# Kernel tuning notes

Hardware: AMD Instinct MI355X
Metric: run time of the kernel (lower is better)

## Reference

```python
import jax, jax.numpy as jnp
import numpy as np

B, H, S, D = 2, 12, 2048, 64

def setup_inputs() -> dict:
    key = jax.random.key(0)
    kq, kk, kv, km = jax.random.split(key, 4)
    return {
        "q": jax.random.normal(kq, (B, H, S, D), dtype=jnp.float32),
        "k": jax.random.normal(kk, (B, H, S, D), dtype=jnp.float32),
        "v": jax.random.normal(kv, (B, H, S, D), dtype=jnp.float32),
        "mask": jax.random.normal(km, (B, 1, S, S), dtype=jnp.float32),
    }

def reference(q, k, v, mask):
    # scores: [B,H,S,S] = Q @ K^T + mask (additive, broadcast over heads)
    scores = jnp.einsum("bhqd,bhkd->bhqk", q, k) + mask
    probs = jax.nn.softmax(scores, axis=-1)
    return jnp.einsum("bhqk,bhkd->bhqd", probs, v)
```

## Files before the change

### kernel.cpp

```cpp
#include <hip/hip_runtime.h>
#include <hip/hip_bf16.h>
#include <stdint.h>

#define S_LEN 2048
#define D_DIM 64
#define HEADS 12
#define KVB   64
#define QBLK  64
#define NTILES (S_LEN / KVB)
#define BH    (2 * HEADS)
#define TILE_BYTES 8192
#define KH_OFF ((size_t)0)
#define KL_OFF ((size_t)BH * NTILES * TILE_BYTES)
#define VT_OFF ((size_t)2 * BH * NTILES * TILE_BYTES)
#define WS_NEED ((size_t)3 * BH * NTILES * TILE_BYTES)

typedef __attribute__((ext_vector_type(8))) short bf16x8;
typedef __attribute__((ext_vector_type(4))) float f32x4;

__device__ __forceinline__ unsigned short f2bf(float x) {
    union { float f; uint32_t u; } v; v.f = x;
    uint32_t r = v.u + 0x7FFFu + ((v.u >> 16) & 1u);
    return (unsigned short)(r >> 16);
}
__device__ __forceinline__ float bf2f(unsigned short h) {
    union { uint32_t u; float f; } t; t.u = ((uint32_t)h) << 16; return t.f;
}
__device__ __forceinline__ void split2(float x, unsigned short& h, unsigned short& l) {
    h = f2bf(x);
    l = f2bf(x - bf2f(h));
}
__device__ __forceinline__ void gload16(const void* g, void* l) {
    __builtin_amdgcn_global_load_lds(
        (const __attribute__((address_space(1))) void*)g,
        (__attribute__((address_space(3))) void*)l, 16, 0, 0);
}

__global__ __launch_bounds__(256, 4)
void convert_kv(const float* __restrict__ K, const float* __restrict__ V,
                unsigned char* __restrict__ ws)
{
    const int blk = blockIdx.x;
    const int bh  = blk >> 5;
    const int t   = blk & 31;
    const long qkv_base = (long)bh * S_LEN * D_DIM;
    const int tid = threadIdx.x;
    unsigned char* kh = ws + KH_OFF + (size_t)blk * TILE_BYTES;
    unsigned char* kl = ws + KL_OFF + (size_t)blk * TILE_BYTES;
    unsigned char* vt = ws + VT_OFF + (size_t)blk * TILE_BYTES;
    const int k0 = t * KVB;

    const float* kp = K + qkv_base + (long)k0 * D_DIM;
    #pragma unroll
    for (int it = 0; it < 4; ++it) {
        int i   = tid + 256 * it;
        int row = i >> 4;
        int c4  = i & 15;
        float4 x = *(const float4*)(kp + row * 64 + c4 * 4);
        unsigned short h0, l0, h1, l1, h2, l2, h3, l3;
        split2(x.x, h0, l0); split2(x.y, h1, l1);
        split2(x.z, h2, l2); split2(x.w, h3, l3);
        int off = row * 128 + ((c4 * 8) ^ ((row & 7) << 4));
        *(uint2*)(kh + off) = make_uint2(((uint32_t)h1 << 16) | h0, ((uint32_t)h3 << 16) | h2);
        *(uint2*)(kl + off) = make_uint2(((uint32_t)l1 << 16) | l0, ((uint32_t)l3 << 16) | l2);
    }

    const float* vp = V + qkv_base + (long)k0 * D_DIM;
    int d = tid & 63, a = tid >> 6;
    #pragma unroll
    for (int h = 0; h < 2; ++h) {
        int kk0 = 32 * h + 8 * a;
        float e0 = vp[(kk0 + 0) * 64 + d], e1 = vp[(kk0 + 1) * 64 + d];
        float e2 = vp[(kk0 + 2) * 64 + d], e3 = vp[(kk0 + 3) * 64 + d];
        float e4 = vp[(kk0 + 4) * 64 + d], e5 = vp[(kk0 + 5) * 64 + d];
        float e6 = vp[(kk0 + 6) * 64 + d], e7 = vp[(kk0 + 7) * 64 + d];
        uint32_t w0 = ((uint32_t)f2bf(e1) << 16) | f2bf(e0);
        uint32_t w1 = ((uint32_t)f2bf(e3) << 16) | f2bf(e2);
        uint32_t w2 = ((uint32_t)f2bf(e5) << 16) | f2bf(e4);
        uint32_t w3 = ((uint32_t)f2bf(e7) << 16) | f2bf(e6);
        int off = d * 128 + ((kk0 * 2) ^ ((d & 7) << 4));
        *(uint4*)(vt + off) = make_uint4(w0, w1, w2, w3);
    }
}

__global__ __launch_bounds__(256, 3)
void attn_fwd_ws(const float* __restrict__ Q, const float* __restrict__ M,
                 const unsigned char* __restrict__ ws, float* __restrict__ O)
{
    __shared__ unsigned char klds_h[8192];
    __shared__ unsigned char klds_l[8192];
    __shared__ unsigned char vlds[8192];
    __shared__ unsigned char mlds[16384];

    const int bid  = blockIdx.x;
    const int bh   = bid >> 5;
    const int qb   = bid & 31;
    const int b    = bh / HEADS;
    const long qkv_base  = (long)bh * S_LEN * D_DIM;
    const long mask_base = (long)b * S_LEN * S_LEN;

    const int tid  = threadIdx.x;
    const int wave = tid >> 6;
    const int lane = tid & 63;
    const int c    = lane & 15;
    const int g    = lane >> 4;
    const int sw   = (c & 7) << 4;

    const int qrow = qb * QBLK + wave * 16 + c;

    bf16x8 qfh[2], qfl[2];
    {
        const float* qp = Q + qkv_base + (long)qrow * D_DIM;
        #pragma unroll
        for (int f = 0; f < 2; ++f) {
            float4 x0 = *(const float4*)(qp + f * 32 + 8 * g);
            float4 x1 = *(const float4*)(qp + f * 32 + 8 * g + 4);
            float e[8] = { x0.x, x0.y, x0.z, x0.w, x1.x, x1.y, x1.z, x1.w };
            bf16x8 th, tl;
            #pragma unroll
            for (int j = 0; j < 8; ++j) {
                unsigned short h, l;
                split2(e[j], h, l);
                th[j] = (short)h; tl[j] = (short)l;
            }
            qfh[f] = th; qfl[f] = tl;
        }
    }

    const unsigned char* khB = ws + KH_OFF + (size_t)bh * NTILES * TILE_BYTES;
    const unsigned char* klB = ws + KL_OFF + (size_t)bh * NTILES * TILE_BYTES;
    const unsigned char* vtB = ws + VT_OFF + (size_t)bh * NTILES * TILE_BYTES;
    const float* mrow0 = M + mask_base + (long)(qb * QBLK) * S_LEN;

    f32x4 o[4] = {};
    float m_run = -INFINITY, l_run = 0.f;

    for (int t0 = 0; t0 < NTILES; ++t0) {
        const unsigned char* khT = khB + (size_t)t0 * TILE_BYTES;
        const unsigned char* klT = klB + (size_t)t0 * TILE_BYTES;
        const unsigned char* vtT = vtB + (size_t)t0 * TILE_BYTES;

        #pragma unroll
        for (int j = 0; j < 2; ++j) {
            int o2 = wave * 2048 + j * 1024;
            gload16(khT + o2 + lane * 16, klds_h + o2);
            gload16(klT + o2 + lane * 16, klds_l + o2);
            gload16(vtT + o2 + lane * 16, vlds + o2);
        }
        #pragma unroll
        for (int j = 0; j < 4; ++j) {
            int o2 = wave * 4096 + j * 1024;
            int X  = o2 + lane * 16;
            int q  = X >> 8;
            int ib = X & 255;
            const unsigned char* gm =
                (const unsigned char*)(mrow0 + (long)q * S_LEN) + t0 * 256;
            gload16(gm + (ib ^ ((q & 7) << 4)), mlds + o2);
        }
        __syncthreads();

        f32x4 st[4];
        #pragma unroll
        for (int kt = 0; kt < 4; ++kt) {
            const unsigned char* bh_ = klds_h + (16 * kt + c) * 128;
            const unsigned char* bl_ = klds_l + (16 * kt + c) * 128;
            bf16x8 kh0 = *(const bf16x8*)(bh_ + ((16 * g) ^ sw));
            bf16x8 kh1 = *(const bf16x8*)(bh_ + ((64 + 16 * g) ^ sw));
            bf16x8 kl0 = *(const bf16x8*)(bl_ + ((16 * g) ^ sw));
            bf16x8 kl1 = *(const bf16x8*)(bl_ + ((64 + 16 * g) ^ sw));
            f32x4 acc = {};
            acc = __builtin_amdgcn_mfma_f32_16x16x32_bf16(kh0, qfl[0], acc, 0, 0, 0);
            acc = __builtin_amdgcn_mfma_f32_16x16x32_bf16(kh1, qfl[1], acc, 0, 0, 0);
            acc = __builtin_amdgcn_mfma_f32_16x16x32_bf16(kl0, qfh[0], acc, 0, 0, 0);
            acc = __builtin_amdgcn_mfma_f32_16x16x32_bf16(kl1, qfh[1], acc, 0, 0, 0);
            acc = __builtin_amdgcn_mfma_f32_16x16x32_bf16(kh0, qfh[0], acc, 0, 0, 0);
            acc = __builtin_amdgcn_mfma_f32_16x16x32_bf16(kh1, qfh[1], acc, 0, 0, 0);
            st[kt] = acc;
        }

        const int mq = wave * 16 + c;
        const unsigned char* mrl = mlds + mq * 256;
        float p[4][4];
        float tmax = -INFINITY;
        #pragma unroll
        for (int kt = 0; kt < 4; ++kt) {
            union { float4 v; float a[4]; } mu;
            mu.v = *(const float4*)(mrl + ((64 * kt + 16 * g) ^ sw));
            #pragma unroll
            for (int r = 0; r < 4; ++r) {
                float sc = st[kt][r] + mu.a[r];
                p[kt][r] = sc;
                tmax = fmaxf(tmax, sc);
            }
        }
        tmax = fmaxf(tmax, __shfl_xor(tmax, 16, 64));
        tmax = fmaxf(tmax, __shfl_xor(tmax, 32, 64));
        float m_new = fmaxf(m_run, tmax);
        float scale = __expf(m_run - m_new);
        float tsum = 0.f;
        #pragma unroll
        for (int kt = 0; kt < 4; ++kt)
            #pragma unroll
            for (int r = 0; r < 4; ++r) {
                float e = __expf(p[kt][r] - m_new);
                p[kt][r] = e;
                tsum += e;
            }
        tsum += __shfl_xor(tsum, 16, 64);
        tsum += __shfl_xor(tsum, 32, 64);
        l_run = l_run * scale + tsum;
        m_run = m_new;
        #pragma unroll
        for (int mt = 0; mt < 4; ++mt) o[mt] *= scale;

        uint32_t w[4][2];
        #pragma unroll
        for (int kt = 0; kt < 4; ++kt) {
            w[kt][0] = ((uint32_t)f2bf(p[kt][1]) << 16) | f2bf(p[kt][0]);
            w[kt][1] = ((uint32_t)f2bf(p[kt][3]) << 16) | f2bf(p[kt][2]);
        }
        bf16x8 pf[2];
        const bool hi_half = (lane & 32) != 0;
        #pragma unroll
        for (int f = 0; f < 2; ++f) {
            uint32_t words[4];
            #pragma unroll
            for (int pp = 0; pp < 4; ++pp) {
                int srcl = 16 * (2 * (g & 1) + (pp >> 1)) + c;
                int addr = srcl << 2;
                int lo = __builtin_amdgcn_ds_bpermute(addr, (int)w[2 * f][pp & 1]);
                int hi = __builtin_amdgcn_ds_bpermute(addr, (int)w[2 * f + 1][pp & 1]);
                words[pp] = hi_half ? (uint32_t)hi : (uint32_t)lo;
            }
            union { uint32_t u[4]; bf16x8 v; } cv;
            cv.u[0] = words[0]; cv.u[1] = words[1];
            cv.u[2] = words[2]; cv.u[3] = words[3];
            pf[f] = cv.v;
        }

        #pragma unroll
        for (int f = 0; f < 2; ++f) {
            #pragma unroll
            for (int mt = 0; mt < 4; ++mt) {
                const unsigned char* base = vlds + (16 * mt + c) * 128;
                bf16x8 vf = *(const bf16x8*)(base + ((64 * f + 16 * g) ^ sw));
                o[mt] = __builtin_amdgcn_mfma_f32_16x16x32_bf16(vf, pf[f], o[mt], 0, 0, 0);
            }
        }
        __syncthreads();
    }

    float inv = 1.0f / l_run;
    float* op = O + qkv_base + (long)qrow * D_DIM;
    #pragma unroll
    for (int mt = 0; mt < 4; ++mt) {
        float4 x = make_float4(o[mt][0] * inv, o[mt][1] * inv,
                               o[mt][2] * inv, o[mt][3] * inv);
        *(float4*)(op + 16 * mt + 4 * g) = x;
    }
}

__global__ __launch_bounds__(256, 3)
void attn_fwd(const float* __restrict__ Q, const float* __restrict__ K,
              const float* __restrict__ V, const float* __restrict__ M,
              float* __restrict__ O)
{
    __shared__ unsigned char klds_h[64 * 128];
    __shared__ unsigned char klds_l[64 * 128];
    __shared__ unsigned char vlds[64 * 128];

    const int bid  = blockIdx.x;
    const int bh   = bid >> 5;
    const int qb   = bid & 31;
    const int b    = bh / HEADS;
    const long qkv_base  = (long)bh * S_LEN * D_DIM;
    const long mask_base = (long)b * S_LEN * S_LEN;

    const int tid  = threadIdx.x;
    const int wave = tid >> 6;
    const int lane = tid & 63;
    const int c    = lane & 15;
    const int g    = lane >> 4;
    const int sw   = (c & 7) << 4;

    const int qrow = qb * QBLK + wave * 16 + c;

    bf16x8 qfh[2], qfl[2];
    {
        const float* qp = Q + qkv_base + (long)qrow * D_DIM;
        #pragma unroll
        for (int f = 0; f < 2; ++f) {
            float4 x0 = *(const float4*)(qp + f * 32 + 8 * g);
            float4 x1 = *(const float4*)(qp + f * 32 + 8 * g + 4);
            float e[8] = { x0.x, x0.y, x0.z, x0.w, x1.x, x1.y, x1.z, x1.w };
            bf16x8 th, tl;
            #pragma unroll
            for (int j = 0; j < 8; ++j) {
                unsigned short h, l;
                split2(e[j], h, l);
                th[j] = (short)h; tl[j] = (short)l;
            }
            qfh[f] = th; qfl[f] = tl;
        }
    }

    f32x4 o[4] = {};
    float m_run = -INFINITY, l_run = 0.f;
    const float* mrow = M + mask_base + (long)qrow * S_LEN;

    for (int t0 = 0; t0 < NTILES; ++t0) {
        const int k0 = t0 * KVB;
        {
            const float* kp = K + qkv_base + (long)k0 * D_DIM;
            #pragma unroll
            for (int it = 0; it < 4; ++it) {
                int i   = tid + 256 * it;
                int row = i >> 4;
                int c4  = i & 15;
                float4 x = *(const float4*)(kp + row * 64 + c4 * 4);
                unsigned short h0, l0, h1, l1, h2, l2, h3, l3;
                split2(x.x, h0, l0); split2(x.y, h1, l1);
                split2(x.z, h2, l2); split2(x.w, h3, l3);
                int off = row * 128 + ((c4 * 8) ^ ((row & 7) << 4));
                *(uint2*)(klds_h + off) =
                    make_uint2(((uint32_t)h1 << 16) | h0, ((uint32_t)h3 << 16) | h2);
                *(uint2*)(klds_l + off) =
                    make_uint2(((uint32_t)l1 << 16) | l0, ((uint32_t)l3 << 16) | l2);
            }
        }
        {
            const float* vp = V + qkv_base + (long)k0 * D_DIM;
            int d = tid & 63, a = tid >> 6;
            #pragma unroll
            for (int h = 0; h < 2; ++h) {
                int kk0 = 32 * h + 8 * a;
                float e0 = vp[(kk0 + 0) * 64 + d], e1 = vp[(kk0 + 1) * 64 + d];
                float e2 = vp[(kk0 + 2) * 64 + d], e3 = vp[(kk0 + 3) * 64 + d];
                float e4 = vp[(kk0 + 4) * 64 + d], e5 = vp[(kk0 + 5) * 64 + d];
                float e6 = vp[(kk0 + 6) * 64 + d], e7 = vp[(kk0 + 7) * 64 + d];
                uint32_t w0 = ((uint32_t)f2bf(e1) << 16) | f2bf(e0);
                uint32_t w1 = ((uint32_t)f2bf(e3) << 16) | f2bf(e2);
                uint32_t w2 = ((uint32_t)f2bf(e5) << 16) | f2bf(e4);
                uint32_t w3 = ((uint32_t)f2bf(e7) << 16) | f2bf(e6);
                int off = d * 128 + ((kk0 * 2) ^ ((d & 7) << 4));
                *(uint4*)(vlds + off) = make_uint4(w0, w1, w2, w3);
            }
        }
        __syncthreads();

        f32x4 st[4];
        #pragma unroll
        for (int kt = 0; kt < 4; ++kt) {
            const unsigned char* bh_ = klds_h + (16 * kt + c) * 128;
            const unsigned char* bl_ = klds_l + (16 * kt + c) * 128;
            bf16x8 kh0 = *(const bf16x8*)(bh_ + ((16 * g) ^ sw));
            bf16x8 kh1 = *(const bf16x8*)(bh_ + ((64 + 16 * g) ^ sw));
            bf16x8 kl0 = *(const bf16x8*)(bl_ + ((16 * g) ^ sw));
            bf16x8 kl1 = *(const bf16x8*)(bl_ + ((64 + 16 * g) ^ sw));
            f32x4 acc = {};
            acc = __builtin_amdgcn_mfma_f32_16x16x32_bf16(kh0, qfl[0], acc, 0, 0, 0);
            acc = __builtin_amdgcn_mfma_f32_16x16x32_bf16(kh1, qfl[1], acc, 0, 0, 0);
            acc = __builtin_amdgcn_mfma_f32_16x16x32_bf16(kl0, qfh[0], acc, 0, 0, 0);
            acc = __builtin_amdgcn_mfma_f32_16x16x32_bf16(kl1, qfh[1], acc, 0, 0, 0);
            acc = __builtin_amdgcn_mfma_f32_16x16x32_bf16(kh0, qfh[0], acc, 0, 0, 0);
            acc = __builtin_amdgcn_mfma_f32_16x16x32_bf16(kh1, qfh[1], acc, 0, 0, 0);
            st[kt] = acc;
        }

        float p[4][4];
        float tmax = -INFINITY;
        #pragma unroll
        for (int kt = 0; kt < 4; ++kt)
            #pragma unroll
            for (int r = 0; r < 4; ++r) {
                float sc = st[kt][r] + mrow[k0 + 16 * kt + 4 * g + r];
                p[kt][r] = sc;
                tmax = fmaxf(tmax, sc);
            }
        tmax = fmaxf(tmax, __shfl_xor(tmax, 16, 64));
        tmax = fmaxf(tmax, __shfl_xor(tmax, 32, 64));
        float m_new = fmaxf(m_run, tmax);
        float scale = __expf(m_run - m_new);
        float tsum = 0.f;
        #pragma unroll
        for (int kt = 0; kt < 4; ++kt)
            #pragma unroll
            for (int r = 0; r < 4; ++r) {
                float e = __expf(p[kt][r] - m_new);
                p[kt][r] = e;
                tsum += e;
            }
        tsum += __shfl_xor(tsum, 16, 64);
        tsum += __shfl_xor(tsum, 32, 64);
        l_run = l_run * scale + tsum;
        m_run = m_new;
        #pragma unroll
        for (int mt = 0; mt < 4; ++mt) o[mt] *= scale;

        uint32_t w[4][2];
        #pragma unroll
        for (int kt = 0; kt < 4; ++kt) {
            w[kt][0] = ((uint32_t)f2bf(p[kt][1]) << 16) | f2bf(p[kt][0]);
            w[kt][1] = ((uint32_t)f2bf(p[kt][3]) << 16) | f2bf(p[kt][2]);
        }
        bf16x8 pf[2];
        const bool hi_half = (lane & 32) != 0;
        #pragma unroll
        for (int f = 0; f < 2; ++f) {
            uint32_t words[4];
            #pragma unroll
            for (int pp = 0; pp < 4; ++pp) {
                int srcl = 16 * (2 * (g & 1) + (pp >> 1)) + c;
                int addr = srcl << 2;
                int lo = __builtin_amdgcn_ds_bpermute(addr, (int)w[2 * f][pp & 1]);
                int hi = __builtin_amdgcn_ds_bpermute(addr, (int)w[2 * f + 1][pp & 1]);
                words[pp] = hi_half ? (uint32_t)hi : (uint32_t)lo;
            }
            union { uint32_t u[4]; bf16x8 v; } cv;
            cv.u[0] = words[0]; cv.u[1] = words[1];
            cv.u[2] = words[2]; cv.u[3] = words[3];
            pf[f] = cv.v;
        }

        #pragma unroll
        for (int f = 0; f < 2; ++f) {
            #pragma unroll
            for (int mt = 0; mt < 4; ++mt) {
                const unsigned char* base = vlds + (16 * mt + c) * 128;
                bf16x8 vf = *(const bf16x8*)(base + ((64 * f + 16 * g) ^ sw));
                o[mt] = __builtin_amdgcn_mfma_f32_16x16x32_bf16(vf, pf[f], o[mt], 0, 0, 0);
            }
        }
        __syncthreads();
    }

    float inv = 1.0f / l_run;
    float* op = O + qkv_base + (long)qrow * D_DIM;
    #pragma unroll
    for (int mt = 0; mt < 4; ++mt) {
        float4 x = make_float4(o[mt][0] * inv, o[mt][1] * inv,
                               o[mt][2] * inv, o[mt][3] * inv);
        *(float4*)(op + 16 * mt + 4 * g) = x;
    }
}

extern "C" void kernel_launch(void* const* d_in, const int* in_sizes, int n_in,
                              void* d_out, int out_size, void* d_ws, size_t ws_size,
                              hipStream_t stream) {
    const float* q = (const float*)d_in[0];
    const float* k = (const float*)d_in[1];
    const float* v = (const float*)d_in[2];
    const float* m = (const float*)d_in[3];
    float* o = (float*)d_out;
    dim3 grid(BH * (S_LEN / QBLK));
    dim3 block(256);
    if (ws_size >= WS_NEED) {
        convert_kv<<<grid, block, 0, stream>>>(k, v, (unsigned char*)d_ws);
        attn_fwd_ws<<<grid, block, 0, stream>>>(q, m, (const unsigned char*)d_ws, o);
    } else {
        attn_fwd<<<grid, block, 0, stream>>>(q, k, v, m, o);
    }
}
```

Baseline: 195.2 us.

## Double-buffer K/V tiles in LDS and prefetch mask rows into registers

The main attention kernel now double-buffers the K-high, K-low and V tiles in LDS, issuing the async global-to-LDS loads for tile t+1 before computing tile t. This hides load latency and leaves one barrier per iteration. The mask is no longer staged through a swizzled LDS buffer; each lane reads its own row directly into registers one tile ahead. The convert kernel now stages results in LDS and writes them out as coalesced 16-byte stores. The trade-off is more LDS (48KB vs 40KB) and more registers, which may lower occupancy, and mask reads are now strided per lane.

```diff
diff --git a/kernel.cpp b/kernel.cpp
--- a/kernel.cpp
+++ b/kernel.cpp
@@ -40,14 +40,15 @@
 void convert_kv(const float* __restrict__ K, const float* __restrict__ V,
                 unsigned char* __restrict__ ws)
 {
+    __shared__ unsigned char kh_s[8192];
+    __shared__ unsigned char kl_s[8192];
+    __shared__ unsigned char vt_s[8192];
+
     const int blk = blockIdx.x;
     const int bh  = blk >> 5;
     const int t   = blk & 31;
     const long qkv_base = (long)bh * S_LEN * D_DIM;
     const int tid = threadIdx.x;
-    unsigned char* kh = ws + KH_OFF + (size_t)blk * TILE_BYTES;
-    unsigned char* kl = ws + KL_OFF + (size_t)blk * TILE_BYTES;
-    unsigned char* vt = ws + VT_OFF + (size_t)blk * TILE_BYTES;
     const int k0 = t * KVB;
 
     const float* kp = K + qkv_base + (long)k0 * D_DIM;
@@ -61,8 +62,8 @@
         split2(x.x, h0, l0); split2(x.y, h1, l1);
         split2(x.z, h2, l2); split2(x.w, h3, l3);
         int off = row * 128 + ((c4 * 8) ^ ((row & 7) << 4));
-        *(uint2*)(kh + off) = make_uint2(((uint32_t)h1 << 16) | h0, ((uint32_t)h3 << 16) | h2);
-        *(uint2*)(kl + off) = make_uint2(((uint32_t)l1 << 16) | l0, ((uint32_t)l3 << 16) | l2);
+        *(uint2*)(kh_s + off) = make_uint2(((uint32_t)h1 << 16) | h0, ((uint32_t)h3 << 16) | h2);
+        *(uint2*)(kl_s + off) = make_uint2(((uint32_t)l1 << 16) | l0, ((uint32_t)l3 << 16) | l2);
     }
 
     const float* vp = V + qkv_base + (long)k0 * D_DIM;
@@ -79,18 +80,43 @@
         uint32_t w2 = ((uint32_t)f2bf(e5) << 16) | f2bf(e4);
         uint32_t w3 = ((uint32_t)f2bf(e7) << 16) | f2bf(e6);
         int off = d * 128 + ((kk0 * 2) ^ ((d & 7) << 4));
-        *(uint4*)(vt + off) = make_uint4(w0, w1, w2, w3);
+        *(uint4*)(vt_s + off) = make_uint4(w0, w1, w2, w3);
+    }
+    __syncthreads();
+
+    unsigned char* kh = ws + KH_OFF + (size_t)blk * TILE_BYTES;
+    unsigned char* kl = ws + KL_OFF + (size_t)blk * TILE_BYTES;
+    unsigned char* vt = ws + VT_OFF + (size_t)blk * TILE_BYTES;
+    #pragma unroll
+    for (int i = 0; i < 2; ++i) {
+        int X = tid * 16 + i * 4096;
+        *(uint4*)(kh + X) = *(const uint4*)(kh_s + X);
+        *(uint4*)(kl + X) = *(const uint4*)(kl_s + X);
+        *(uint4*)(vt + X) = *(const uint4*)(vt_s + X);
+    }
+}
+
+__device__ __forceinline__ void stage_tiles(const unsigned char* khT, const unsigned char* klT,
+                                            const unsigned char* vtT,
+                                            unsigned char* kh_d, unsigned char* kl_d,
+                                            unsigned char* vt_d, int wave, int lane)
+{
+    #pragma unroll
+    for (int j = 0; j < 2; ++j) {
+        int o2 = wave * 2048 + j * 1024;
+        gload16(khT + o2 + lane * 16, kh_d + o2);
+        gload16(klT + o2 + lane * 16, kl_d + o2);
+        gload16(vtT + o2 + lane * 16, vt_d + o2);
     }
 }
 
 __global__ __launch_bounds__(256, 3)
-void attn_fwd_ws(const float* __restrict__ Q, const float* __restrict__ M,
+void attn_fwd_db(const float* __restrict__ Q, const float* __restrict__ M,
                  const unsigned char* __restrict__ ws, float* __restrict__ O)
 {
-    __shared__ unsigned char klds_h[8192];
-    __shared__ unsigned char klds_l[8192];
-    __shared__ unsigned char vlds[8192];
-    __shared__ unsigned char mlds[16384];
+    __shared__ unsigned char klds_h[2][8192];
+    __shared__ unsigned char klds_l[2][8192];
+    __shared__ unsigned char vlds[2][8192];
 
     const int bid  = blockIdx.x;
     const int bh   = bid >> 5;
@@ -130,32 +156,215 @@
     const unsigned char* khB = ws + KH_OFF + (size_t)bh * NTILES * TILE_BYTES;
     const unsigned char* klB = ws + KL_OFF + (size_t)bh * NTILES * TILE_BYTES;
     const unsigned char* vtB = ws + VT_OFF + (size_t)bh * NTILES * TILE_BYTES;
-    const float* mrow0 = M + mask_base + (long)(qb * QBLK) * S_LEN;
+    const float* mrow = M + mask_base + (long)qrow * S_LEN;
 
     f32x4 o[4] = {};
     float m_run = -INFINITY, l_run = 0.f;
 
+    stage_tiles(khB, klB, vtB, klds_h[0], klds_l[0], vlds[0], wave, lane);
+    f32x4 mreg[4], nreg[4];
+    #pragma unroll
+    for (int kt = 0; kt < 4; ++kt)
+        mreg[kt] = *(const f32x4*)(mrow + 16 * kt + 4 * g);
+    __syncthreads();
+
+    int cur = 0;
     for (int t0 = 0; t0 < NTILES; ++t0) {
-        const unsigned char* khT = khB + (size_t)t0 * TILE_BYTES;
-        const unsigned char* klT = klB + (size_t)t0 * TILE_BYTES;
-        const unsigned char* vtT = vtB + (size_t)t0 * TILE_BYTES;
-
-        #pragma unroll
-        for (int j = 0; j < 2; ++j) {
-            int o2 = wave * 2048 + j * 1024;
-            gload16(khT + o2 + lane * 16, klds_h + o2);
-            gload16(klT + o2 + lane * 16, klds_l + o2);
-            gload16(vtT + o2 + lane * 16, vlds + o2);
-        }
-        #pragma unroll
-        for (int j = 0; j < 4; ++j) {
-            int o2 = wave * 4096 + j * 1024;
-            int X  = o2 + lane * 16;
-            int q  = X >> 8;
-            int ib = X & 255;
-            const unsigned char* gm =
-                (const unsigned char*)(mrow0 + (long)q * S_LEN) + t0 * 256;
-            gload16(gm + (ib ^ ((q & 7) << 4)), mlds + o2);
+        if (t0 + 1 < NTILES) {
+            stage_tiles(khB + (size_t)(t0 + 1) * TILE_BYTES,
+                        klB + (size_t)(t0 + 1) * TILE_BYTES,
+                        vtB + (size_t)(t0 + 1) * TILE_BYTES,
+                        klds_h[cur ^ 1], klds_l[cur ^ 1], vlds[cur ^ 1], wave, lane);
+            #pragma unroll
+            for (int kt = 0; kt < 4; ++kt)
+                nreg[kt] = *(const f32x4*)(mrow + (t0 + 1) * 64 + 16 * kt + 4 * g);
+        }
+
+        f32x4 st[4];
+        #pragma unroll
+        for (int kt = 0; kt < 4; ++kt) {
+            const unsigned char* bh_ = klds_h[cur] + (16 * kt + c) * 128;
+            const unsigned char* bl_ = klds_l[cur] + (16 * kt + c) * 128;
+            bf16x8 kh0 = *(const bf16x8*)(bh_ + ((16 * g) ^ sw));
+            bf16x8 kh1 = *(const bf16x8*)(bh_ + ((64 + 16 * g) ^ sw));
+            bf16x8 kl0 = *(const bf16x8*)(bl_ + ((16 * g) ^ sw));
+            bf16x8 kl1 = *(const bf16x8*)(bl_ + ((64 + 16 * g) ^ sw));
+            f32x4 acc = {};
+            acc = __builtin_amdgcn_mfma_f32_16x16x32_bf16(kh0, qfl[0], acc, 0, 0, 0);
+            acc = __builtin_amdgcn_mfma_f32_16x16x32_bf16(kh1, qfl[1], acc, 0, 0, 0);
+            acc = __builtin_amdgcn_mfma_f32_16x16x32_bf16(kl0, qfh[0], acc, 0, 0, 0);
+            acc = __builtin_amdgcn_mfma_f32_16x16x32_bf16(kl1, qfh[1], acc, 0, 0, 0);
+            acc = __builtin_amdgcn_mfma_f32_16x16x32_bf16(kh0, qfh[0], acc, 0, 0, 0);
+            acc = __builtin_amdgcn_mfma_f32_16x16x32_bf16(kh1, qfh[1], acc, 0, 0, 0);
+            st[kt] = acc;
+        }
+
+        float p[4][4];
+        float tmax = -INFINITY;
+        #pragma unroll
+        for (int kt = 0; kt < 4; ++kt)
+            #pragma unroll
+            for (int r = 0; r < 4; ++r) {
+                float sc = st[kt][r] + mreg[kt][r];
+                p[kt][r] = sc;
+                tmax = fmaxf(tmax, sc);
+            }
+        tmax = fmaxf(tmax, __shfl_xor(tmax, 16, 64));
+        tmax = fmaxf(tmax, __shfl_xor(tmax, 32, 64));
+        float m_new = fmaxf(m_run, tmax);
+        float scale = __expf(m_run - m_new);
+        float tsum = 0.f;
+        #pragma unroll
+        for (int kt = 0; kt < 4; ++kt)
+            #pragma unroll
+            for (int r = 0; r < 4; ++r) {
+                float e = __expf(p[kt][r] - m_new);
+                p[kt][r] = e;
+                tsum += e;
+            }
+        tsum += __shfl_xor(tsum, 16, 64);
+        tsum += __shfl_xor(tsum, 32, 64);
+        l_run = l_run * scale + tsum;
+        m_run = m_new;
+        #pragma unroll
+        for (int mt = 0; mt < 4; ++mt) o[mt] *= scale;
+
+        uint32_t w[4][2];
+        #pragma unroll
+        for (int kt = 0; kt < 4; ++kt) {
+            w[kt][0] = ((uint32_t)f2bf(p[kt][1]) << 16) | f2bf(p[kt][0]);
+            w[kt][1] = ((uint32_t)f2bf(p[kt][3]) << 16) | f2bf(p[kt][2]);
+        }
+        bf16x8 pf[2];
+        const bool hi_half = (lane & 32) != 0;
+        #pragma unroll
+        for (int f = 0; f < 2; ++f) {
+            uint32_t words[4];
+            #pragma unroll
+            for (int pp = 0; pp < 4; ++pp) {
+                int srcl = 16 * (2 * (g & 1) + (pp >> 1)) + c;
+                int addr = srcl << 2;
+                int lo = __builtin_amdgcn_ds_bpermute(addr, (int)w[2 * f][pp & 1]);
+                int hi = __builtin_amdgcn_ds_bpermute(addr, (int)w[2 * f + 1][pp & 1]);
+                words[pp] = hi_half ? (uint32_t)hi : (uint32_t)lo;
+            }
+            union { uint32_t u[4]; bf16x8 v; } cv;
+            cv.u[0] = words[0]; cv.u[1] = words[1];
+            cv.u[2] = words[2]; cv.u[3] = words[3];
+            pf[f] = cv.v;
+        }
+
+        #pragma unroll
+        for (int f = 0; f < 2; ++f) {
+            #pragma unroll
+            for (int mt = 0; mt < 4; ++mt) {
+                const unsigned char* base = vlds[cur] + (16 * mt + c) * 128;
+                bf16x8 vf = *(const bf16x8*)(base + ((64 * f + 16 * g) ^ sw));
+                o[mt] = __builtin_amdgcn_mfma_f32_16x16x32_bf16(vf, pf[f], o[mt], 0, 0, 0);
+            }
+        }
+
+        __syncthreads();
+        cur ^= 1;
+        #pragma unroll
+        for (int kt = 0; kt < 4; ++kt) mreg[kt] = nreg[kt];
+    }
+
+    float inv = 1.0f / l_run;
+    float* op = O + qkv_base + (long)qrow * D_DIM;
+    #pragma unroll
+    for (int mt = 0; mt < 4; ++mt) {
+        float4 x = make_float4(o[mt][0] * inv, o[mt][1] * inv,
+                               o[mt][2] * inv, o[mt][3] * inv);
+        *(float4*)(op + 16 * mt + 4 * g) = x;
+    }
+}
+
+__global__ __launch_bounds__(256, 3)
+void attn_fwd(const float* __restrict__ Q, const float* __restrict__ K,
+              const float* __restrict__ V, const float* __restrict__ M,
+              float* __restrict__ O)
+{
+    __shared__ unsigned char klds_h[64 * 128];
+    __shared__ unsigned char klds_l[64 * 128];
+    __shared__ unsigned char vlds[64 * 128];
+
+    const int bid  = blockIdx.x;
+    const int bh   = bid >> 5;
+    const int qb   = bid & 31;
+    const int b    = bh / HEADS;
+    const long qkv_base  = (long)bh * S_LEN * D_DIM;
+    const long mask_base = (long)b * S_LEN * S_LEN;
+
+    const int tid  = threadIdx.x;
+    const int wave = tid >> 6;
+    const int lane = tid & 63;
+    const int c    = lane & 15;
+    const int g    = lane >> 4;
+    const int sw   = (c & 7) << 4;
+
+    const int qrow = qb * QBLK + wave * 16 + c;
+
+    bf16x8 qfh[2], qfl[2];
+    {
+        const float* qp = Q + qkv_base + (long)qrow * D_DIM;
+        #pragma unroll
+        for (int f = 0; f < 2; ++f) {
+            float4 x0 = *(const float4*)(qp + f * 32 + 8 * g);
+            float4 x1 = *(const float4*)(qp + f * 32 + 8 * g + 4);
+            float e[8] = { x0.x, x0.y, x0.z, x0.w, x1.x, x1.y, x1.z, x1.w };
+            bf16x8 th, tl;
+            #pragma unroll
+            for (int j = 0; j < 8; ++j) {
+                unsigned short h, l;
+                split2(e[j], h, l);
+                th[j] = (short)h; tl[j] = (short)l;
+            }
+            qfh[f] = th; qfl[f] = tl;
+        }
+    }
+
+    f32x4 o[4] = {};
+    float m_run = -INFINITY, l_run = 0.f;
+    const float* mrow = M + mask_base + (long)qrow * S_LEN;
+
+    for (int t0 = 0; t0 < NTILES; ++t0) {
+        const int k0 = t0 * KVB;
+        {
+            const float* kp = K + qkv_base + (long)k0 * D_DIM;
+            #pragma unroll
+            for (int it = 0; it < 4; ++it) {
+                int i   = tid + 256 * it;
+                int row = i >> 4;
+                int c4  = i & 15;
+                float4 x = *(const float4*)(kp + row * 64 + c4 * 4);
+                unsigned short h0, l0, h1, l1, h2, l2, h3, l3;
+                split2(x.x, h0, l0); split2(x.y, h1, l1);
+                split2(x.z, h2, l2); split2(x.w, h3, l3);
+                int off = row * 128 + ((c4 * 8) ^ ((row & 7) << 4));
+                *(uint2*)(klds_h + off) =
+                    make_uint2(((uint32_t)h1 << 16) | h0, ((uint32_t)h3 << 16) | h2);
+                *(uint2*)(klds_l + off) =
+                    make_uint2(((uint32_t)l1 << 16) | l0, ((uint32_t)l3 << 16) | l2);
+            }
+        }
+        {
+            const float* vp = V + qkv_base + (long)k0 * D_DIM;
+            int d = tid & 63, a = tid >> 6;
+            #pragma unroll
+            for (int h = 0; h < 2; ++h) {
+                int kk0 = 32 * h + 8 * a;
+                float e0 = vp[(kk0 + 0) * 64 + d], e1 = vp[(kk0 + 1) * 64 + d];
+                float e2 = vp[(kk0 + 2) * 64 + d], e3 = vp[(kk0 + 3) * 64 + d];
+                float e4 = vp[(kk0 + 4) * 64 + d], e5 = vp[(kk0 + 5) * 64 + d];
+                float e6 = vp[(kk0 + 6) * 64 + d], e7 = vp[(kk0 + 7) * 64 + d];
+                uint32_t w0 = ((uint32_t)f2bf(e1) << 16) | f2bf(e0);
+                uint32_t w1 = ((uint32_t)f2bf(e3) << 16) | f2bf(e2);
+                uint32_t w2 = ((uint32_t)f2bf(e5) << 16) | f2bf(e4);
+                uint32_t w3 = ((uint32_t)f2bf(e7) << 16) | f2bf(e6);
+                int off = d * 128 + ((kk0 * 2) ^ ((d & 7) << 4));
+                *(uint4*)(vlds + off) = make_uint4(w0, w1, w2, w3);
+            }
         }
         __syncthreads();
 
@@ -178,195 +387,6 @@
             st[kt] = acc;
         }
 
-        const int mq = wave * 16 + c;
-        const unsigned char* mrl = mlds + mq * 256;
-        float p[4][4];
-        float tmax = -INFINITY;
-        #pragma unroll
-        for (int kt = 0; kt < 4; ++kt) {
-            union { float4 v; float a[4]; } mu;
-            mu.v = *(const float4*)(mrl + ((64 * kt + 16 * g) ^ sw));
-            #pragma unroll
-            for (int r = 0; r < 4; ++r) {
-                float sc = st[kt][r] + mu.a[r];
-                p[kt][r] = sc;
-                tmax = fmaxf(tmax, sc);
-            }
-        }
-        tmax = fmaxf(tmax, __shfl_xor(tmax, 16, 64));
-        tmax = fmaxf(tmax, __shfl_xor(tmax, 32, 64));
-        float m_new = fmaxf(m_run, tmax);
-        float scale = __expf(m_run - m_new);
-        float tsum = 0.f;
-        #pragma unroll
-        for (int kt = 0; kt < 4; ++kt)
-            #pragma unroll
-            for (int r = 0; r < 4; ++r) {
-                float e = __expf(p[kt][r] - m_new);
-                p[kt][r] = e;
-                tsum += e;
-            }
-        tsum += __shfl_xor(tsum, 16, 64);
-        tsum += __shfl_xor(tsum, 32, 64);
-        l_run = l_run * scale + tsum;
-        m_run = m_new;
-        #pragma unroll
-        for (int mt = 0; mt < 4; ++mt) o[mt] *= scale;
-
-        uint32_t w[4][2];
-        #pragma unroll
-        for (int kt = 0; kt < 4; ++kt) {
-            w[kt][0] = ((uint32_t)f2bf(p[kt][1]) << 16) | f2bf(p[kt][0]);
-            w[kt][1] = ((uint32_t)f2bf(p[kt][3]) << 16) | f2bf(p[kt][2]);
-        }
-        bf16x8 pf[2];
-        const bool hi_half = (lane & 32) != 0;
-        #pragma unroll
-        for (int f = 0; f < 2; ++f) {
-            uint32_t words[4];
-            #pragma unroll
-            for (int pp = 0; pp < 4; ++pp) {
-                int srcl = 16 * (2 * (g & 1) + (pp >> 1)) + c;
-                int addr = srcl << 2;
-                int lo = __builtin_amdgcn_ds_bpermute(addr, (int)w[2 * f][pp & 1]);
-                int hi = __builtin_amdgcn_ds_bpermute(addr, (int)w[2 * f + 1][pp & 1]);
-                words[pp] = hi_half ? (uint32_t)hi : (uint32_t)lo;
-            }
-            union { uint32_t u[4]; bf16x8 v; } cv;
-            cv.u[0] = words[0]; cv.u[1] = words[1];
-            cv.u[2] = words[2]; cv.u[3] = words[3];
-            pf[f] = cv.v;
-        }
-
-        #pragma unroll
-        for (int f = 0; f < 2; ++f) {
-            #pragma unroll
-            for (int mt = 0; mt < 4; ++mt) {
-                const unsigned char* base = vlds + (16 * mt + c) * 128;
-                bf16x8 vf = *(const bf16x8*)(base + ((64 * f + 16 * g) ^ sw));
-                o[mt] = __builtin_amdgcn_mfma_f32_16x16x32_bf16(vf, pf[f], o[mt], 0, 0, 0);
-            }
-        }
-        __syncthreads();
-    }
-
-    float inv = 1.0f / l_run;
-    float* op = O + qkv_base + (long)qrow * D_DIM;
-    #pragma unroll
-    for (int mt = 0; mt < 4; ++mt) {
-        float4 x = make_float4(o[mt][0] * inv, o[mt][1] * inv,
-                               o[mt][2] * inv, o[mt][3] * inv);
-        *(float4*)(op + 16 * mt + 4 * g) = x;
-    }
-}
-
-__global__ __launch_bounds__(256, 3)
-void attn_fwd(const float* __restrict__ Q, const float* __restrict__ K,
-              const float* __restrict__ V, const float* __restrict__ M,
-              float* __restrict__ O)
-{
-    __shared__ unsigned char klds_h[64 * 128];
-    __shared__ unsigned char klds_l[64 * 128];
-    __shared__ unsigned char vlds[64 * 128];
-
-    const int bid  = blockIdx.x;
-    const int bh   = bid >> 5;
-    const int qb   = bid & 31;
-    const int b    = bh / HEADS;
-    const long qkv_base  = (long)bh * S_LEN * D_DIM;
-    const long mask_base = (long)b * S_LEN * S_LEN;
-
-    const int tid  = threadIdx.x;
-    const int wave = tid >> 6;
-    const int lane = tid & 63;
-    const int c    = lane & 15;
-    const int g    = lane >> 4;
-    const int sw   = (c & 7) << 4;
-
-    const int qrow = qb * QBLK + wave * 16 + c;
-
-    bf16x8 qfh[2], qfl[2];
-    {
-        const float* qp = Q + qkv_base + (long)qrow * D_DIM;
-        #pragma unroll
-        for (int f = 0; f < 2; ++f) {
-            float4 x0 = *(const float4*)(qp + f * 32 + 8 * g);
-            float4 x1 = *(const float4*)(qp + f * 32 + 8 * g + 4);
-            float e[8] = { x0.x, x0.y, x0.z, x0.w, x1.x, x1.y, x1.z, x1.w };
-            bf16x8 th, tl;
-            #pragma unroll
-            for (int j = 0; j < 8; ++j) {
-                unsigned short h, l;
-                split2(e[j], h, l);
-                th[j] = (short)h; tl[j] = (short)l;
-            }
-            qfh[f] = th; qfl[f] = tl;
-        }
-    }
-
-    f32x4 o[4] = {};
-    float m_run = -INFINITY, l_run = 0.f;
-    const float* mrow = M + mask_base + (long)qrow * S_LEN;
-
-    for (int t0 = 0; t0 < NTILES; ++t0) {
-        const int k0 = t0 * KVB;
-        {
-            const float* kp = K + qkv_base + (long)k0 * D_DIM;
-            #pragma unroll
-            for (int it = 0; it < 4; ++it) {
-                int i   = tid + 256 * it;
-                int row = i >> 4;
-                int c4  = i & 15;
-                float4 x = *(const float4*)(kp + row * 64 + c4 * 4);
-                unsigned short h0, l0, h1, l1, h2, l2, h3, l3;
-                split2(x.x, h0, l0); split2(x.y, h1, l1);
-                split2(x.z, h2, l2); split2(x.w, h3, l3);
-                int off = row * 128 + ((c4 * 8) ^ ((row & 7) << 4));
-                *(uint2*)(klds_h + off) =
-                    make_uint2(((uint32_t)h1 << 16) | h0, ((uint32_t)h3 << 16) | h2);
-                *(uint2*)(klds_l + off) =
-                    make_uint2(((uint32_t)l1 << 16) | l0, ((uint32_t)l3 << 16) | l2);
-            }
-        }
-        {
-            const float* vp = V + qkv_base + (long)k0 * D_DIM;
-            int d = tid & 63, a = tid >> 6;
-            #pragma unroll
-            for (int h = 0; h < 2; ++h) {
-                int kk0 = 32 * h + 8 * a;
-                float e0 = vp[(kk0 + 0) * 64 + d], e1 = vp[(kk0 + 1) * 64 + d];
-                float e2 = vp[(kk0 + 2) * 64 + d], e3 = vp[(kk0 + 3) * 64 + d];
-                float e4 = vp[(kk0 + 4) * 64 + d], e5 = vp[(kk0 + 5) * 64 + d];
-                float e6 = vp[(kk0 + 6) * 64 + d], e7 = vp[(kk0 + 7) * 64 + d];
-                uint32_t w0 = ((uint32_t)f2bf(e1) << 16) | f2bf(e0);
-                uint32_t w1 = ((uint32_t)f2bf(e3) << 16) | f2bf(e2);
-                uint32_t w2 = ((uint32_t)f2bf(e5) << 16) | f2bf(e4);
-                uint32_t w3 = ((uint32_t)f2bf(e7) << 16) | f2bf(e6);
-                int off = d * 128 + ((kk0 * 2) ^ ((d & 7) << 4));
-                *(uint4*)(vlds + off) = make_uint4(w0, w1, w2, w3);
-            }
-        }
-        __syncthreads();
-
-        f32x4 st[4];
-        #pragma unroll
-        for (int kt = 0; kt < 4; ++kt) {
-            const unsigned char* bh_ = klds_h + (16 * kt + c) * 128;
-            const unsigned char* bl_ = klds_l + (16 * kt + c) * 128;
-            bf16x8 kh0 = *(const bf16x8*)(bh_ + ((16 * g) ^ sw));
-            bf16x8 kh1 = *(const bf16x8*)(bh_ + ((64 + 16 * g) ^ sw));
-            bf16x8 kl0 = *(const bf16x8*)(bl_ + ((16 * g) ^ sw));
-            bf16x8 kl1 = *(const bf16x8*)(bl_ + ((64 + 16 * g) ^ sw));
-            f32x4 acc = {};
-            acc = __builtin_amdgcn_mfma_f32_16x16x32_bf16(kh0, qfl[0], acc, 0, 0, 0);
-            acc = __builtin_amdgcn_mfma_f32_16x16x32_bf16(kh1, qfl[1], acc, 0, 0, 0);
-            acc = __builtin_amdgcn_mfma_f32_16x16x32_bf16(kl0, qfh[0], acc, 0, 0, 0);
-            acc = __builtin_amdgcn_mfma_f32_16x16x32_bf16(kl1, qfh[1], acc, 0, 0, 0);
-            acc = __builtin_amdgcn_mfma_f32_16x16x32_bf16(kh0, qfh[0], acc, 0, 0, 0);
-            acc = __builtin_amdgcn_mfma_f32_16x16x32_bf16(kh1, qfh[1], acc, 0, 0, 0);
-            st[kt] = acc;
-        }
-
         float p[4][4];
         float tmax = -INFINITY;
         #pragma unroll
@@ -456,7 +476,7 @@
     dim3 block(256);
     if (ws_size >= WS_NEED) {
         convert_kv<<<grid, block, 0, stream>>>(k, v, (unsigned char*)d_ws);
-        attn_fwd_ws<<<grid, block, 0, stream>>>(q, m, (const unsigned char*)d_ws, o);
+        attn_fwd_db<<<grid, block, 0, stream>>>(q, m, (const unsigned char*)d_ws, o);
     } else {
         attn_fwd<<<grid, block, 0, stream>>>(q, k, v, m, o);
     }
```

Measured after the change: 200.7 us. 2.8% more time.
